# Performance work log

Measured on AMD Instinct MI355X. Metric: run time of the kernel, lower is better.

Reference implementation:

```python
import jax, jax.numpy as jnp
import numpy as np

D_MODEL = 2048
NUM_HEADS = 16
D_K = D_MODEL // NUM_HEADS
B, S = 2, 2048


def setup_inputs() -> dict:
    key = jax.random.key(0)
    ks = jax.random.split(key, 9)
    sc = 1.0 / np.sqrt(D_MODEL)
    x = jax.random.normal(ks[0], (B, S, D_MODEL), dtype=jnp.float32)
    # broadcastable causal mask [1,1,S,S]; mask==0 positions get -inf
    mask = jnp.tril(jnp.ones((S, S), dtype=jnp.int32))[None, None]
    wq = jax.random.normal(ks[1], (D_MODEL, D_MODEL), dtype=jnp.float32) * sc
    bq = jax.random.normal(ks[2], (D_MODEL,), dtype=jnp.float32) * 0.01
    wk = jax.random.normal(ks[3], (D_MODEL, D_MODEL), dtype=jnp.float32) * sc
    bk = jax.random.normal(ks[4], (D_MODEL,), dtype=jnp.float32) * 0.01
    wv = jax.random.normal(ks[5], (D_MODEL, D_MODEL), dtype=jnp.float32) * sc
    bv = jax.random.normal(ks[6], (D_MODEL,), dtype=jnp.float32) * 0.01
    wo = jax.random.normal(ks[7], (D_MODEL, D_MODEL), dtype=jnp.float32) * sc
    bo = jax.random.normal(ks[8], (D_MODEL,), dtype=jnp.float32) * 0.01
    return {"x": x, "wq": wq, "bq": bq, "wk": wk, "bk": bk,
            "wv": wv, "bv": bv, "wo": wo, "bo": bo, "mask": mask}


def reference(x, wq, bq, wk, bk, wv, bv, wo, bo, mask):
    b, s, _ = x.shape
    # nn.Linear computes x @ W.T + b; weights stored [out, in]
    def proj(w, bias):
        y = jnp.einsum('bsd,ed->bse', x, w) + bias
        return y.reshape(b, s, NUM_HEADS, D_K).transpose(0, 2, 1, 3)  # [b,h,s,dk]
    q = proj(wq, bq)
    k = proj(wk, bk)
    v = proj(wv, bv)
    scores = jnp.einsum('bhid,bhjd->bhij', q, k) / jnp.sqrt(jnp.float32(D_K))
    scores = jnp.where(mask == 0, -jnp.inf, scores)
    attn = jax.nn.softmax(scores, axis=-1)  # dropout p=0.0 -> identity
    out = jnp.einsum('bhij,bhjd->bhid', attn, v)
    out = out.transpose(0, 2, 1, 3).reshape(b, s, D_MODEL)
    return jnp.einsum('bsd,ed->bse', out, wo) + bo
```

## Files before the change

### kernel.cpp

```cpp
#include <hip/hip_runtime.h>
#include <cstdint>
#include <cstddef>

typedef __attribute__((ext_vector_type(8))) short bf16x8;
typedef __attribute__((ext_vector_type(8))) unsigned short u16x8;
typedef __attribute__((ext_vector_type(4))) unsigned short u16x4;
typedef __attribute__((ext_vector_type(4))) float f32x4;

#define MFMA16(A, B, C) __builtin_amdgcn_mfma_f32_16x16x32_bf16((A), (B), (C), 0, 0, 0)

__device__ __forceinline__ unsigned short f2bf(float f) {
  unsigned u = __builtin_bit_cast(unsigned, f);
  u += 0x7FFFu + ((u >> 16) & 1u);
  return (unsigned short)(u >> 16);
}

__device__ __forceinline__ void gload_lds16(const void* gsrc, void* ldst) {
  __builtin_amdgcn_global_load_lds(
      (const __attribute__((address_space(1))) unsigned int*)gsrc,
      (__attribute__((address_space(3))) unsigned int*)ldst,
      16, 0, 0);
}

__global__ __launch_bounds__(256) void cvt_all(
    const float* __restrict__ sx, const float* __restrict__ s1,
    const float* __restrict__ s2, const float* __restrict__ s3,
    const float* __restrict__ s4,
    unsigned short* __restrict__ dx, unsigned short* __restrict__ d1,
    unsigned short* __restrict__ d2, unsigned short* __restrict__ d3,
    unsigned short* __restrict__ d4) {
  const int y = blockIdx.y;
  const float* src;
  unsigned short* dst;
  if (y == 0)      { src = sx;               dst = dx; }
  else if (y == 1) { src = sx + (1u << 22);  dst = dx + (1u << 22); }
  else if (y == 2) { src = s1; dst = d1; }
  else if (y == 3) { src = s2; dst = d2; }
  else if (y == 4) { src = s3; dst = d3; }
  else             { src = s4; dst = d4; }
  const size_t i = ((size_t)blockIdx.x * 256 + threadIdx.x) * 4;
  f32x4 v = *(const f32x4*)(src + i);
  u16x4 o;
  o[0] = f2bf(v[0]); o[1] = f2bf(v[1]); o[2] = f2bf(v[2]); o[3] = f2bf(v[3]);
  *(u16x4*)(dst + i) = o;
}

template <int MODE>
__device__ __forceinline__ void gemm8_tile(const unsigned short* __restrict__ A,
                                           const unsigned short* __restrict__ W,
                                           const float* __restrict__ bias,
                                           void* __restrict__ C,
                                           int bx, int by) {
  constexpr int K = 2048, N = 2048;
  constexpr int NT = K / 64;
  __shared__ unsigned short lA[3][256 * 64];
  __shared__ unsigned short lB[3][128 * 64];
  const int tid = threadIdx.x;
  const int lane = tid & 63;
  const int w = tid >> 6;
  const int g = lane >> 4;
  const int l15 = lane & 15;
  const int wm = w >> 1, wn = w & 1;
  const int m0 = by * 256, n0 = bx * 128;

  auto stageA = [&](int kt, int buf) {
    const int kb = kt * 64;
#pragma unroll
    for (int it = 0; it < 4; ++it) {
      const int f = it * 512 + tid;
      const int r = f >> 3, s = f & 7;
      gload_lds16(A + (size_t)(m0 + r) * K + kb + ((s * 8) ^ ((r & 7) << 3)),
                  (char*)&lA[buf][0] + (it * 512 + w * 64) * 16);
    }
  };
  auto stageB = [&](int kt, int buf) {
    const int kb = kt * 64;
#pragma unroll
    for (int it = 0; it < 2; ++it) {
      const int f = it * 512 + tid;
      const int r = f >> 3, s = f & 7;
      gload_lds16(W + (size_t)(n0 + r) * K + kb + ((s * 8) ^ ((r & 7) << 3)),
                  (char*)&lB[buf][0] + (it * 512 + w * 64) * 16);
    }
  };

  f32x4 acc[4][4];
#pragma unroll
  for (int i = 0; i < 4; ++i)
#pragma unroll
    for (int j = 0; j < 4; ++j) acc[i][j] = f32x4{0.f, 0.f, 0.f, 0.f};

  stageA(0, 0); stageB(0, 0);
  stageA(1, 1); stageB(1, 1);
  asm volatile("s_waitcnt vmcnt(6)" ::: "memory");
  __builtin_amdgcn_s_barrier();
  __builtin_amdgcn_sched_barrier(0);

  int cur = 0, nxt = 2;
  for (int kt = 0; kt < NT; ++kt) {
    const unsigned short* As = &lA[cur][0];
    const unsigned short* Bs = &lB[cur][0];
    bf16x8 bfr[4][2], af[2][2];
#pragma unroll
    for (int ni = 0; ni < 4; ++ni) {
      const int rb = wn * 64 + ni * 16 + l15;
#pragma unroll
      for (int kh = 0; kh < 2; ++kh)
        bfr[ni][kh] =
            *(const bf16x8*)&Bs[rb * 64 + ((kh * 32 + g * 8) ^ ((rb & 7) << 3))];
    }
#pragma unroll
    for (int mi = 0; mi < 2; ++mi) {
      const int ra = wm * 64 + mi * 16 + l15;
#pragma unroll
      for (int kh = 0; kh < 2; ++kh)
        af[mi][kh] =
            *(const bf16x8*)&As[ra * 64 + ((kh * 32 + g * 8) ^ ((ra & 7) << 3))];
    }
    if (kt + 2 < NT) stageA(kt + 2, nxt);
    __builtin_amdgcn_s_barrier();
    __builtin_amdgcn_sched_barrier(0);
    __builtin_amdgcn_s_setprio(1);
#pragma unroll
    for (int kh = 0; kh < 2; ++kh)
#pragma unroll
      for (int mi = 0; mi < 2; ++mi)
#pragma unroll
        for (int ni = 0; ni < 4; ++ni)
          acc[mi][ni] = MFMA16(af[mi][kh], bfr[ni][kh], acc[mi][ni]);
    __builtin_amdgcn_s_setprio(0);
    __builtin_amdgcn_s_barrier();
    __builtin_amdgcn_sched_barrier(0);
#pragma unroll
    for (int mi = 0; mi < 2; ++mi) {
      const int ra = wm * 64 + (mi + 2) * 16 + l15;
#pragma unroll
      for (int kh = 0; kh < 2; ++kh)
        af[mi][kh] =
            *(const bf16x8*)&As[ra * 64 + ((kh * 32 + g * 8) ^ ((ra & 7) << 3))];
    }
    if (kt + 2 < NT) stageB(kt + 2, nxt);
    __builtin_amdgcn_s_barrier();
    __builtin_amdgcn_sched_barrier(0);
    __builtin_amdgcn_s_setprio(1);
#pragma unroll
    for (int kh = 0; kh < 2; ++kh)
#pragma unroll
      for (int mi = 0; mi < 2; ++mi)
#pragma unroll
        for (int ni = 0; ni < 4; ++ni)
          acc[mi + 2][ni] = MFMA16(af[mi][kh], bfr[ni][kh], acc[mi + 2][ni]);
    __builtin_amdgcn_s_setprio(0);
    if (kt < NT - 2)       asm volatile("s_waitcnt vmcnt(6)" ::: "memory");
    else if (kt == NT - 2) asm volatile("s_waitcnt vmcnt(0)" ::: "memory");
    __builtin_amdgcn_s_barrier();
    __builtin_amdgcn_sched_barrier(0);
    cur = (cur == 2) ? 0 : cur + 1;
    nxt = (nxt == 2) ? 0 : nxt + 1;
  }

#pragma unroll
  for (int ni = 0; ni < 4; ++ni) {
    const int n = n0 + wn * 64 + ni * 16 + l15;
    const float bval = bias[n];
#pragma unroll
    for (int mi = 0; mi < 4; ++mi) {
      const int mb = m0 + wm * 64 + mi * 16 + g * 4;
#pragma unroll
      for (int r = 0; r < 4; ++r) {
        const int m = mb + r;
        const float fv = acc[mi][ni][r] + bval;
        if (MODE == 0) {
          ((float*)C)[(size_t)m * N + n] = fv;
        } else {
          const int bb = m >> 11, ss = m & 2047, hh = n >> 7, dk = n & 127;
          ((unsigned short*)C)[(((size_t)(bb * 16 + hh) * 2048) + ss) * 128 + dk] =
              f2bf(fv);
        }
      }
    }
  }
}

__global__ __launch_bounds__(512, 2) void gemm_qkv(
    const unsigned short* __restrict__ x,
    const unsigned short* __restrict__ wq, const float* __restrict__ bq,
    const unsigned short* __restrict__ wk, const float* __restrict__ bk,
    const unsigned short* __restrict__ wv, const float* __restrict__ bv,
    unsigned short* __restrict__ qo, unsigned short* __restrict__ ko,
    unsigned short* __restrict__ vo) {
  const int z = blockIdx.z;
  const unsigned short* W = (z == 0) ? wq : (z == 1) ? wk : wv;
  const float* B = (z == 0) ? bq : (z == 1) ? bk : bv;
  unsigned short* O = (z == 0) ? qo : (z == 1) ? ko : vo;
  gemm8_tile<1>(x, W, B, O, blockIdx.x, blockIdx.y);
}

__global__ __launch_bounds__(512, 2) void gemm_out(
    const unsigned short* __restrict__ A, const unsigned short* __restrict__ wo,
    const float* __restrict__ bo, float* __restrict__ C) {
  gemm8_tile<0>(A, wo, bo, C, blockIdx.x, blockIdx.y);
}

__global__ __launch_bounds__(256, 2) void attn_fwd(
    const unsigned short* __restrict__ Q, const unsigned short* __restrict__ K,
    const unsigned short* __restrict__ V, unsigned short* __restrict__ O) {
  __shared__ unsigned short lK[2][64 * 128];
  __shared__ unsigned short lV[128 * 72];
  __shared__ unsigned short lP[4][32 * 72];
  const int tid = threadIdx.x;
  const int lane = tid & 63;
  const int w = tid >> 6;
  const int g = lane >> 4;
  const int l15 = lane & 15;
  const int bx = blockIdx.x;
  const int bh = blockIdx.y;
  const int qb = (bh >= 16) ? (15 - bx) : bx;
  const int nt = 2 * qb + 2;
  const size_t head_off = (size_t)bh * 2048 * 128;
  const unsigned short* Qh = Q + head_off;
  const unsigned short* Kh = K + head_off;
  const unsigned short* Vh = V + head_off;

  bf16x8 qf[2][4];
#pragma unroll
  for (int mi = 0; mi < 2; ++mi) {
    const int row = qb * 128 + w * 32 + mi * 16 + l15;
#pragma unroll
    for (int ks = 0; ks < 4; ++ks) {
      const int s = ks * 4 + g;
      qf[mi][ks] = *(const bf16x8*)(Qh + (size_t)row * 128 + s * 8);
    }
  }

  const int vj0 = (tid & 31) * 2;
  const int vd0 = (tid >> 5) * 16;
  u16x8 vr[4];

  auto stageK = [&](int t, int buf) {
#pragma unroll
    for (int it = 0; it < 4; ++it) {
      const int f = it * 256 + tid;
      const int r = f >> 4, s = f & 15;
      const int sc = s ^ (r & 7);
      gload_lds16(Kh + (size_t)(t * 64 + r) * 128 + sc * 8,
                  (char*)&lK[buf][0] + (it * 256 + w * 64) * 16);
    }
  };
  auto loadV = [&](int t) {
    const unsigned short* vp = Vh + (size_t)(t * 64 + vj0) * 128 + vd0;
    vr[0] = *(const u16x8*)(vp);
    vr[1] = *(const u16x8*)(vp + 8);
    vr[2] = *(const u16x8*)(vp + 128);
    vr[3] = *(const u16x8*)(vp + 136);
  };
  auto writeV = [&]() {
#pragma unroll
    for (int dd = 0; dd < 8; ++dd) {
      unsigned pk0 = (unsigned)vr[0][dd] | ((unsigned)vr[2][dd] << 16);
      unsigned pk1 = (unsigned)vr[1][dd] | ((unsigned)vr[3][dd] << 16);
      *(unsigned*)&lV[(vd0 + dd) * 72 + vj0] = pk0;
      *(unsigned*)&lV[(vd0 + 8 + dd) * 72 + vj0] = pk1;
    }
  };

  loadV(0);
  stageK(0, 0);
  writeV();
  __syncthreads();

  f32x4 acc_o[2][8];
#pragma unroll
  for (int mi = 0; mi < 2; ++mi)
#pragma unroll
    for (int i = 0; i < 8; ++i) acc_o[mi][i] = f32x4{0.f, 0.f, 0.f, 0.f};
  float mrun[2], lrun[2];
#pragma unroll
  for (int mi = 0; mi < 2; ++mi) { mrun[mi] = -__builtin_inff(); lrun[mi] = 0.f; }

  const float SL2E = 0.12751744f;
  const int qrow0 = qb * 128 + w * 32;

  int cur = 0;
  for (int t = 0; t < nt; ++t) {
    const int kv0 = t * 64;
    const bool pre = (t + 1 < nt);
    if (pre) { loadV(t + 1); stageK(t + 1, cur ^ 1); }

    const bool active = (kv0 <= qrow0 + 31);
    if (active) {
      const unsigned short* lKc = &lK[cur][0];
      f32x4 sacc[4][2];
#pragma unroll
      for (int jb = 0; jb < 4; ++jb) {
        sacc[jb][0] = f32x4{0.f, 0.f, 0.f, 0.f};
        sacc[jb][1] = f32x4{0.f, 0.f, 0.f, 0.f};
      }
      __builtin_amdgcn_s_setprio(1);
#pragma unroll
      for (int jb = 0; jb < 4; ++jb) {
        const int r = jb * 16 + l15;
#pragma unroll
        for (int ks = 0; ks < 4; ++ks) {
          const int s = ks * 4 + g;
          bf16x8 kf = *(const bf16x8*)&lKc[r * 128 + (s ^ (r & 7)) * 8];
          sacc[jb][0] = MFMA16(kf, qf[0][ks], sacc[jb][0]);
          sacc[jb][1] = MFMA16(kf, qf[1][ks], sacc[jb][1]);
        }
      }
      __builtin_amdgcn_s_setprio(0);

      const bool need_mask = (kv0 + 63 >= qrow0);
      float psc_l[2];
#pragma unroll
      for (int mi = 0; mi < 2; ++mi) {
        const int icol = qrow0 + mi * 16 + l15;
        f32x4 pe[4];
#pragma unroll
        for (int jb = 0; jb < 4; ++jb) {
#pragma unroll
          for (int rr = 0; rr < 4; ++rr) {
            float tv = sacc[jb][mi][rr] * SL2E;
            if (need_mask && (kv0 + jb * 16 + g * 4 + rr > icol))
              tv = -__builtin_inff();
            pe[jb][rr] = tv;
          }
        }
        f32x4 m4 = f32x4{fmaxf(fmaxf(pe[0][0], pe[1][0]), fmaxf(pe[2][0], pe[3][0])),
                         fmaxf(fmaxf(pe[0][1], pe[1][1]), fmaxf(pe[2][1], pe[3][1])),
                         fmaxf(fmaxf(pe[0][2], pe[1][2]), fmaxf(pe[2][2], pe[3][2])),
                         fmaxf(fmaxf(pe[0][3], pe[1][3]), fmaxf(pe[2][3], pe[3][3]))};
        float mx = fmaxf(fmaxf(m4[0], m4[1]), fmaxf(m4[2], m4[3]));
        mx = fmaxf(mx, __shfl_xor(mx, 16));
        mx = fmaxf(mx, __shfl_xor(mx, 32));
        const float mnew = fmaxf(mrun[mi], mx);
        psc_l[mi] = exp2f(mrun[mi] - mnew);
        mrun[mi] = mnew;
        float rs = 0.f;
#pragma unroll
        for (int jb = 0; jb < 4; ++jb) {
#pragma unroll
          for (int rr = 0; rr < 4; ++rr) {
            const float e = exp2f(pe[jb][rr] - mnew);
            pe[jb][rr] = e;
            rs += e;
          }
        }
        rs += __shfl_xor(rs, 16);
        rs += __shfl_xor(rs, 32);
        lrun[mi] = lrun[mi] * psc_l[mi] + rs;
#pragma unroll
        for (int jb = 0; jb < 4; ++jb)
#pragma unroll
          for (int rr = 0; rr < 4; ++rr)
            lP[w][(mi * 16 + l15) * 72 + jb * 16 + g * 4 + rr] = f2bf(pe[jb][rr]);
      }
      __builtin_amdgcn_sched_barrier(0);

      float psc_pv[2][4];
#pragma unroll
      for (int mi = 0; mi < 2; ++mi)
#pragma unroll
        for (int r = 0; r < 4; ++r)
          psc_pv[mi][r] = __shfl(psc_l[mi], g * 4 + r);
#pragma unroll
      for (int mi = 0; mi < 2; ++mi)
#pragma unroll
        for (int nb = 0; nb < 8; ++nb)
#pragma unroll
          for (int r = 0; r < 4; ++r) acc_o[mi][nb][r] *= psc_pv[mi][r];

      bf16x8 pa[2][2];
#pragma unroll
      for (int mi = 0; mi < 2; ++mi)
#pragma unroll
        for (int h = 0; h < 2; ++h)
          pa[mi][h] = *(const bf16x8*)&lP[w][(mi * 16 + l15) * 72 + h * 32 + g * 8];
      __builtin_amdgcn_s_setprio(1);
#pragma unroll
      for (int nb = 0; nb < 8; ++nb) {
        const int vrow = nb * 16 + l15;
#pragma unroll
        for (int h = 0; h < 2; ++h) {
          bf16x8 vf = *(const bf16x8*)&lV[vrow * 72 + h * 32 + g * 8];
          acc_o[0][nb] = MFMA16(pa[0][h], vf, acc_o[0][nb]);
          acc_o[1][nb] = MFMA16(pa[1][h], vf, acc_o[1][nb]);
        }
      }
      __builtin_amdgcn_s_setprio(0);
    }

    __syncthreads();
    if (pre) writeV();
    __syncthreads();
    cur ^= 1;
  }

  const int b = bh >> 4, hh = bh & 15;
  float linv[2][4];
#pragma unroll
  for (int mi = 0; mi < 2; ++mi)
#pragma unroll
    for (int r = 0; r < 4; ++r)
      linv[mi][r] = 1.0f / __shfl(lrun[mi], g * 4 + r);
#pragma unroll
  for (int mi = 0; mi < 2; ++mi)
#pragma unroll
    for (int nb = 0; nb < 8; ++nb)
#pragma unroll
      for (int r = 0; r < 4; ++r) {
        const int i = qb * 128 + w * 32 + mi * 16 + g * 4 + r;
        const float o = acc_o[mi][nb][r] * linv[mi][r];
        O[((size_t)(b * 2048 + i)) * 2048 + hh * 128 + nb * 16 + l15] = f2bf(o);
      }
}

extern "C" void kernel_launch(void* const* d_in, const int* in_sizes, int n_in,
                              void* d_out, int out_size, void* d_ws, size_t ws_size,
                              hipStream_t stream) {
  const float* x  = (const float*)d_in[0];
  const float* wq = (const float*)d_in[1];
  const float* bq = (const float*)d_in[2];
  const float* wk = (const float*)d_in[3];
  const float* bk = (const float*)d_in[4];
  const float* wv = (const float*)d_in[5];
  const float* bv = (const float*)d_in[6];
  const float* wo = (const float*)d_in[7];
  const float* bo = (const float*)d_in[8];

  const size_t NX = (size_t)2 * 2048 * 2048;
  const size_t NW = (size_t)2048 * 2048;
  const size_t need = (NX + 4 * NW + 3 * NX) * sizeof(unsigned short);
  if (ws_size < need) return;
  unsigned short* xbf  = (unsigned short*)d_ws;
  unsigned short* wqb  = xbf + NX;
  unsigned short* wkb  = wqb + NW;
  unsigned short* wvb  = wkb + NW;
  unsigned short* wob  = wvb + NW;
  unsigned short* qbuf = wob + NW;
  unsigned short* kbuf = qbuf + NX;
  unsigned short* vbuf = kbuf + NX;
  unsigned short* aobuf = xbf;

  cvt_all<<<dim3(4096, 6), 256, 0, stream>>>(x, wq, wk, wv, wo,
                                             xbf, wqb, wkb, wvb, wob);
  gemm_qkv<<<dim3(16, 16, 3), 512, 0, stream>>>(xbf, wqb, bq, wkb, bk, wvb, bv,
                                                qbuf, kbuf, vbuf);
  attn_fwd<<<dim3(16, 32), 256, 0, stream>>>(qbuf, kbuf, vbuf, aobuf);
  gemm_out<<<dim3(16, 16), 512, 0, stream>>>(aobuf, wob, bo, (float*)d_out);
}
```

Measured before the change: 292.0 us.

## Widen GEMM tiles to 256x256 with double buffering and XCD-aware block remap

The projection GEMMs now use 256x256 output tiles, with each wave computing 128x64, in place of 256x128. This halves the grid and raises arithmetic intensity per LDS load. The three-stage staggered pipeline becomes a simpler double buffer: each iteration issues the next tile's loads up front, then waits for all loads with a full vmcnt(0) barrier. Block indices are remapped from a 1D grid so that neighbouring tiles land on the same XCD for L2 reuse. The risks are less latency hiding from the shallower pipeline, more register pressure from 32 accumulators, and only 128 blocks for the output GEMM, which may underfill the 256 CUs.

```diff
diff --git a/kernel.cpp b/kernel.cpp
--- a/kernel.cpp
+++ b/kernel.cpp
@@ -46,22 +46,22 @@
 }
 
 template <int MODE>
-__device__ __forceinline__ void gemm8_tile(const unsigned short* __restrict__ A,
+__device__ __forceinline__ void gemmw_tile(const unsigned short* __restrict__ A,
                                            const unsigned short* __restrict__ W,
                                            const float* __restrict__ bias,
                                            void* __restrict__ C,
                                            int bx, int by) {
   constexpr int K = 2048, N = 2048;
   constexpr int NT = K / 64;
-  __shared__ unsigned short lA[3][256 * 64];
-  __shared__ unsigned short lB[3][128 * 64];
+  __shared__ unsigned short lA[2][256 * 64];
+  __shared__ unsigned short lB[2][256 * 64];
   const int tid = threadIdx.x;
   const int lane = tid & 63;
   const int w = tid >> 6;
   const int g = lane >> 4;
   const int l15 = lane & 15;
-  const int wm = w >> 1, wn = w & 1;
-  const int m0 = by * 256, n0 = bx * 128;
+  const int wm = w >> 2, wn = w & 3;
+  const int m0 = by * 256, n0 = bx * 256;
 
   auto stageA = [&](int kt, int buf) {
     const int kb = kt * 64;
@@ -76,7 +76,7 @@
   auto stageB = [&](int kt, int buf) {
     const int kb = kt * 64;
 #pragma unroll
-    for (int it = 0; it < 2; ++it) {
+    for (int it = 0; it < 4; ++it) {
       const int f = it * 512 + tid;
       const int r = f >> 3, s = f & 7;
       gload_lds16(W + (size_t)(n0 + r) * K + kb + ((s * 8) ^ ((r & 7) << 3)),
@@ -84,79 +84,48 @@
     }
   };
 
-  f32x4 acc[4][4];
-#pragma unroll
-  for (int i = 0; i < 4; ++i)
+  f32x4 acc[8][4];
+#pragma unroll
+  for (int i = 0; i < 8; ++i)
 #pragma unroll
     for (int j = 0; j < 4; ++j) acc[i][j] = f32x4{0.f, 0.f, 0.f, 0.f};
 
   stageA(0, 0); stageB(0, 0);
-  stageA(1, 1); stageB(1, 1);
-  asm volatile("s_waitcnt vmcnt(6)" ::: "memory");
+  asm volatile("s_waitcnt vmcnt(0)" ::: "memory");
   __builtin_amdgcn_s_barrier();
   __builtin_amdgcn_sched_barrier(0);
 
-  int cur = 0, nxt = 2;
   for (int kt = 0; kt < NT; ++kt) {
+    const int cur = kt & 1;
+    if (kt + 1 < NT) { stageA(kt + 1, cur ^ 1); stageB(kt + 1, cur ^ 1); }
     const unsigned short* As = &lA[cur][0];
     const unsigned short* Bs = &lB[cur][0];
-    bf16x8 bfr[4][2], af[2][2];
-#pragma unroll
-    for (int ni = 0; ni < 4; ++ni) {
-      const int rb = wn * 64 + ni * 16 + l15;
-#pragma unroll
-      for (int kh = 0; kh < 2; ++kh)
-        bfr[ni][kh] =
+#pragma unroll
+    for (int kh = 0; kh < 2; ++kh) {
+      bf16x8 bfr[4], af[8];
+#pragma unroll
+      for (int ni = 0; ni < 4; ++ni) {
+        const int rb = wn * 64 + ni * 16 + l15;
+        bfr[ni] =
             *(const bf16x8*)&Bs[rb * 64 + ((kh * 32 + g * 8) ^ ((rb & 7) << 3))];
-    }
-#pragma unroll
-    for (int mi = 0; mi < 2; ++mi) {
-      const int ra = wm * 64 + mi * 16 + l15;
-#pragma unroll
-      for (int kh = 0; kh < 2; ++kh)
-        af[mi][kh] =
+      }
+#pragma unroll
+      for (int mi = 0; mi < 8; ++mi) {
+        const int ra = wm * 128 + mi * 16 + l15;
+        af[mi] =
             *(const bf16x8*)&As[ra * 64 + ((kh * 32 + g * 8) ^ ((ra & 7) << 3))];
-    }
-    if (kt + 2 < NT) stageA(kt + 2, nxt);
+      }
+      __builtin_amdgcn_s_setprio(1);
+#pragma unroll
+      for (int mi = 0; mi < 8; ++mi)
+#pragma unroll
+        for (int ni = 0; ni < 4; ++ni)
+          acc[mi][ni] = MFMA16(af[mi], bfr[ni], acc[mi][ni]);
+      __builtin_amdgcn_s_setprio(0);
+    }
+    asm volatile("s_waitcnt vmcnt(0) lgkmcnt(0)" ::: "memory");
     __builtin_amdgcn_s_barrier();
     __builtin_amdgcn_sched_barrier(0);
-    __builtin_amdgcn_s_setprio(1);
-#pragma unroll
-    for (int kh = 0; kh < 2; ++kh)
-#pragma unroll
-      for (int mi = 0; mi < 2; ++mi)
-#pragma unroll
-        for (int ni = 0; ni < 4; ++ni)
-          acc[mi][ni] = MFMA16(af[mi][kh], bfr[ni][kh], acc[mi][ni]);
-    __builtin_amdgcn_s_setprio(0);
-    __builtin_amdgcn_s_barrier();
-    __builtin_amdgcn_sched_barrier(0);
-#pragma unroll
-    for (int mi = 0; mi < 2; ++mi) {
-      const int ra = wm * 64 + (mi + 2) * 16 + l15;
-#pragma unroll
-      for (int kh = 0; kh < 2; ++kh)
-        af[mi][kh] =
-            *(const bf16x8*)&As[ra * 64 + ((kh * 32 + g * 8) ^ ((ra & 7) << 3))];
-    }
-    if (kt + 2 < NT) stageB(kt + 2, nxt);
-    __builtin_amdgcn_s_barrier();
-    __builtin_amdgcn_sched_barrier(0);
-    __builtin_amdgcn_s_setprio(1);
-#pragma unroll
-    for (int kh = 0; kh < 2; ++kh)
-#pragma unroll
-      for (int mi = 0; mi < 2; ++mi)
-#pragma unroll
-        for (int ni = 0; ni < 4; ++ni)
-          acc[mi + 2][ni] = MFMA16(af[mi][kh], bfr[ni][kh], acc[mi + 2][ni]);
-    __builtin_amdgcn_s_setprio(0);
-    if (kt < NT - 2)       asm volatile("s_waitcnt vmcnt(6)" ::: "memory");
-    else if (kt == NT - 2) asm volatile("s_waitcnt vmcnt(0)" ::: "memory");
-    __builtin_amdgcn_s_barrier();
-    __builtin_amdgcn_sched_barrier(0);
-    cur = (cur == 2) ? 0 : cur + 1;
-    nxt = (nxt == 2) ? 0 : nxt + 1;
   }
 
 #pragma unroll
@@ -164,8 +133,8 @@
     const int n = n0 + wn * 64 + ni * 16 + l15;
     const float bval = bias[n];
 #pragma unroll
-    for (int mi = 0; mi < 4; ++mi) {
-      const int mb = m0 + wm * 64 + mi * 16 + g * 4;
+    for (int mi = 0; mi < 8; ++mi) {
+      const int mb = m0 + wm * 128 + mi * 16 + g * 4;
 #pragma unroll
       for (int r = 0; r < 4; ++r) {
         const int m = mb + r;
@@ -189,17 +158,26 @@
     const unsigned short* __restrict__ wv, const float* __restrict__ bv,
     unsigned short* __restrict__ qo, unsigned short* __restrict__ ko,
     unsigned short* __restrict__ vo) {
-  const int z = blockIdx.z;
+  const int o = blockIdx.x;
+  const int t = (o & 7) * 48 + (o >> 3);
+  const int by = t / 24;
+  const int c = t - by * 24;
+  const int z = c >> 3;
+  const int bx = c & 7;
   const unsigned short* W = (z == 0) ? wq : (z == 1) ? wk : wv;
   const float* B = (z == 0) ? bq : (z == 1) ? bk : bv;
   unsigned short* O = (z == 0) ? qo : (z == 1) ? ko : vo;
-  gemm8_tile<1>(x, W, B, O, blockIdx.x, blockIdx.y);
+  gemmw_tile<1>(x, W, B, O, bx, by);
 }
 
 __global__ __launch_bounds__(512, 2) void gemm_out(
     const unsigned short* __restrict__ A, const unsigned short* __restrict__ wo,
     const float* __restrict__ bo, float* __restrict__ C) {
-  gemm8_tile<0>(A, wo, bo, C, blockIdx.x, blockIdx.y);
+  const int o = blockIdx.x;
+  const int t = (o & 7) * 16 + (o >> 3);
+  const int by = t >> 3;
+  const int bx = t & 7;
+  gemmw_tile<0>(A, wo, bo, C, bx, by);
 }
 
 __global__ __launch_bounds__(256, 2) void attn_fwd(
@@ -444,8 +422,8 @@
 
   cvt_all<<<dim3(4096, 6), 256, 0, stream>>>(x, wq, wk, wv, wo,
                                              xbf, wqb, wkb, wvb, wob);
-  gemm_qkv<<<dim3(16, 16, 3), 512, 0, stream>>>(xbf, wqb, bq, wkb, bk, wvb, bv,
-                                                qbuf, kbuf, vbuf);
+  gemm_qkv<<<dim3(384), 512, 0, stream>>>(xbf, wqb, bq, wkb, bk, wvb, bv,
+                                          qbuf, kbuf, vbuf);
   attn_fwd<<<dim3(16, 32), 256, 0, stream>>>(qbuf, kbuf, vbuf, aobuf);
-  gemm_out<<<dim3(16, 16), 512, 0, stream>>>(aobuf, wob, bo, (float*)d_out);
-}
+  gemm_out<<<dim3(128), 512, 0, stream>>>(aobuf, wob, bo, (float*)d_out);
+}
```

New measurement: 335.3 us. +14.8%, slower.
